# Kernel optimization log

Hardware: AMD Instinct MI355X
Metric: run time of the kernel (lower is better)

The kernel has to match this reference:

```python
import jax, jax.numpy as jnp
import numpy as np

BLOCK = 192
SCALE = 2048 ** (-0.5)


def setup_inputs() -> dict:
    key = jax.random.key(0)
    k1, k2, k3, k4 = jax.random.split(key, 4)
    B, N, C = 8, 1920, 512
    x = jax.random.normal(k1, (B, N, C), dtype=jnp.float32)
    g = jax.random.normal(k2, (B, N, C), dtype=jnp.float32)
    # nn.Linear(dim, dim, bias=False) weights, stored as [out, in] like torch
    Wq = jax.random.normal(k3, (C, C), dtype=jnp.float32) * (1.0 / np.sqrt(C))
    Wg = jax.random.normal(k4, (C, C), dtype=jnp.float32) * (1.0 / np.sqrt(C))
    return {"x": x, "g": g, "Wq": Wq, "Wg": Wg}


def reference(x, g, Wq, Wg):
    B, N, C = g.shape
    # q = x + mean over tokens of g
    q = x + jnp.mean(g, axis=1, keepdims=True)
    rel_q = jnp.einsum('bnc,dc->bnd', q, Wq)  # Linear: y = x @ W^T
    # ---- block-local cosine attention over chunks of 192 tokens ----
    gb = g.reshape(B * N // BLOCK, BLOCK, C)
    norm = jnp.linalg.norm(gb, axis=-1, keepdims=True)
    rel = gb / jnp.maximum(norm, 1e-12)  # F.normalize(dim=-1)
    scores = jnp.einsum('bic,bjc->bij', rel, rel) * SCALE  # [nb,192,192]
    attn = jax.nn.softmax(scores, axis=-1)
    g2 = jnp.einsum('bij,bjc->bic', attn, gb).reshape(B, N, C)
    # ---- global cross attention ----
    rel_g = jnp.einsum('bnc,dc->bnd', g2, Wg)
    scores2 = jnp.einsum('bmc,bnc->bmn', rel_q, rel_g) * SCALE  # [B,M,N]
    attn2 = jax.nn.softmax(scores2, axis=-1)
    out = jnp.einsum('bmn,bnc->bmc', attn2, g2)
    return out
```

## Files before the change

kernel.cpp:

```cpp
#include <hip/hip_runtime.h>
#include <math.h>

constexpr int Bsz  = 8;
constexpr int Ntok = 1920;
constexpr int Cdim = 512;
constexpr int BLK  = 192;
constexpr int Mrows = Bsz * Ntok;
constexpr int NBLK  = Mrows / BLK;
constexpr float SCALE = 0.02209708691207961f;

typedef _Float16 half8 __attribute__((ext_vector_type(8)));
typedef float    f32x4 __attribute__((ext_vector_type(4)));

#define GLOAD_LDS16(gp, lp) __builtin_amdgcn_global_load_lds( \
    (const __attribute__((address_space(1))) void*)(gp),      \
    (__attribute__((address_space(3))) void*)(lp), 16, 0, 0)

__device__ inline unsigned short f2h(float f) {
    _Float16 h = (_Float16)f;
    return __builtin_bit_cast(unsigned short, h);
}
__device__ inline float h2f(unsigned short u) {
    return (float)__builtin_bit_cast(_Float16, u);
}

template<int BK> __device__ inline int smask(int r) {
    return (BK == 32) ? ((r & 3) ^ ((r >> 2) & 3)) : (r & 7);
}

template<int N> __device__ __forceinline__ void vm_wait() {
    if constexpr (N == 0)      asm volatile("s_waitcnt vmcnt(0)" ::: "memory");
    else if constexpr (N == 2) asm volatile("s_waitcnt vmcnt(2)" ::: "memory");
    else if constexpr (N == 4) asm volatile("s_waitcnt vmcnt(4)" ::: "memory");
    else if constexpr (N == 6) asm volatile("s_waitcnt vmcnt(6)" ::: "memory");
    else                       asm volatile("s_waitcnt vmcnt(8)" ::: "memory");
}

__global__ __launch_bounds__(256) void prep_g(
    const float* __restrict__ g, unsigned short* __restrict__ gh,
    float* __restrict__ invn)
{
    int wid = threadIdx.x >> 6, lane = threadIdx.x & 63;
    int row = blockIdx.x * 4 + wid;
    const float* p = g + (size_t)row * Cdim + lane * 8;
    float4 v0 = *(const float4*)p;
    float4 v1 = *(const float4*)(p + 4);
    float ss = v0.x * v0.x + v0.y * v0.y + v0.z * v0.z + v0.w * v0.w
             + v1.x * v1.x + v1.y * v1.y + v1.z * v1.z + v1.w * v1.w;
    #pragma unroll
    for (int o = 1; o < 64; o <<= 1) ss += __shfl_xor(ss, o);
    if (lane == 0) invn[row] = 1.0f / fmaxf(sqrtf(ss), 1e-12f);
    ushort4 h0, h1;
    h0.x = f2h(v0.x); h0.y = f2h(v0.y); h0.z = f2h(v0.z); h0.w = f2h(v0.w);
    h1.x = f2h(v1.x); h1.y = f2h(v1.y); h1.z = f2h(v1.z); h1.w = f2h(v1.w);
    ushort4* d = (ushort4*)(gh + (size_t)row * Cdim + lane * 8);
    d[0] = h0; d[1] = h1;
}

__global__ void mean_partial(const unsigned short* __restrict__ gh, float* __restrict__ part) {
    int b = blockIdx.x, t = blockIdx.y, c = threadIdx.x;
    const unsigned short* p = gh + ((size_t)b * Ntok + (size_t)t * 48) * Cdim + c;
    float s = 0.f;
    #pragma unroll 4
    for (int n = 0; n < 48; ++n) s += h2f(p[(size_t)n * Cdim]);
    part[((size_t)b * 40 + t) * Cdim + c] = s;
}

__global__ void mean_final(const float* __restrict__ part, float* __restrict__ meang) {
    int b = blockIdx.x, c = threadIdx.x;
    float s = 0.f;
    for (int t = 0; t < 40; ++t) s += part[((size_t)b * 40 + t) * Cdim + c];
    meang[b * Cdim + c] = s * (1.0f / (float)Ntok);
}

__global__ void cvt_k(const float* __restrict__ src, const float* __restrict__ bias,
                      unsigned short* __restrict__ dst, int n4) {
    int i = blockIdx.x * 256 + threadIdx.x;
    if (i >= n4) return;
    float4 v = ((const float4*)src)[i];
    if (bias) {
        int b  = i / (Ntok * Cdim / 4);
        int c4 = (i & (Cdim / 4 - 1)) << 2;
        float4 bv = *(const float4*)&bias[b * Cdim + c4];
        v.x += bv.x; v.y += bv.y; v.z += bv.z; v.w += bv.w;
    }
    ushort4 h;
    h.x = f2h(v.x); h.y = f2h(v.y); h.z = f2h(v.z); h.w = f2h(v.w);
    ((ushort4*)dst)[i] = h;
}

__global__ __launch_bounds__(256) void transpose1(
    const unsigned short* __restrict__ in, unsigned short* __restrict__ out,
    int R, int C, long inB, long outB)
{
    int z = blockIdx.z;
    in  += (size_t)z * inB;
    out += (size_t)z * outB;
    __shared__ unsigned short th[64][68];
    int r0 = blockIdx.y * 64, c0 = blockIdx.x * 64;
    int tr = threadIdx.x >> 4, tc = (threadIdx.x & 15) * 4;
    for (int rr = tr; rr < 64; rr += 16) {
        ushort4 h = *(const ushort4*)&in[(size_t)(r0 + rr) * C + c0 + tc];
        th[tc + 0][rr] = h.x; th[tc + 1][rr] = h.y; th[tc + 2][rr] = h.z; th[tc + 3][rr] = h.w;
    }
    __syncthreads();
    for (int cc = tr; cc < 64; cc += 16) {
        ushort4 h = *(const ushort4*)&th[cc][tc];
        *(ushort4*)&out[(size_t)(c0 + cc) * R + r0 + tc] = h;
    }
}

template<int FM, int FN, int BK>
__global__ __launch_bounds__(256) void mfma_gemm(
    const unsigned short* __restrict__ A, const unsigned short* __restrict__ B,
    float* __restrict__ Of32, unsigned short* __restrict__ Oh,
    int N, int K, int ld,
    long aB, long bB, long oB,
    float alpha, const float* __restrict__ rs, const float* __restrict__ cs, int sB,
    float* __restrict__ psum, int pM, int pSlots)
{
    constexpr int BM = FM * 32, BN = FN * 32;
    constexpr int RPC = 512 / BK;
    constexpr int LPR = BK / 8;
    constexpr int NCH = (BM + BN) / RPC;
    constexpr int CPW = NCH / 4;
    int z = blockIdx.z;

    int gx = gridDim.x;
    int nwg = gx * gridDim.y;
    int orig = blockIdx.y * gx + blockIdx.x;
    int q = nwg >> 3, r = nwg & 7;
    int xcd = orig & 7, idx = orig >> 3;
    int wgid = (xcd < r ? xcd * (q + 1) : r * (q + 1) + (xcd - r) * q) + idx;
    int bx = wgid % gx;
    int m0 = (wgid / gx) * BM, n0 = bx * BN;

    __shared__ __align__(16) unsigned short As[2][BM * BK];
    __shared__ __align__(16) unsigned short Bs[2][BN * BK];

    int tid  = threadIdx.x;
    int lane = tid & 63, wid = tid >> 6;
    int wm = (wid >> 1) * (FM * 16), wn = (wid & 1) * (FN * 16);

    int srow = lane / LPR;
    int sgc  = (lane % LPR) ^ smask<BK>(srow);

    const unsigned short* csrc[CPW];
    unsigned short* cdst0[CPW];
    unsigned short* cdst1[CPW];
    #pragma unroll
    for (int i = 0; i < CPW; ++i) {
        int c = wid * CPW + i;
        if (c < BM / RPC) {
            csrc[i]  = A + (size_t)z * aB + (size_t)(m0 + c * RPC + srow) * ld + sgc * 8;
            cdst0[i] = &As[0][c * 512];
            cdst1[i] = &As[1][c * 512];
        } else {
            int cb = c - BM / RPC;
            csrc[i]  = B + (size_t)z * bB + (size_t)(n0 + cb * RPC + srow) * ld + sgc * 8;
            cdst0[i] = &Bs[0][cb * 512];
            cdst1[i] = &Bs[1][cb * 512];
        }
    }

    f32x4 acc[FM][FN] = {};
    int fr = lane & 15, kq = lane >> 4;

    const int nt = K / BK;
    #pragma unroll
    for (int i = 0; i < CPW; ++i) GLOAD_LDS16(csrc[i], cdst0[i]);
    #pragma unroll
    for (int i = 0; i < CPW; ++i) GLOAD_LDS16(csrc[i] + BK, cdst1[i]);

    for (int t = 0; t < nt; ++t) {
        int cur = t & 1;
        if (t + 1 < nt) vm_wait<CPW>(); else vm_wait<0>();
        __builtin_amdgcn_sched_barrier(0);
        __builtin_amdgcn_s_barrier();
        __builtin_amdgcn_sched_barrier(0);

        const unsigned short* Ab = As[cur];
        const unsigned short* Bb = Bs[cur];
        #pragma unroll
        for (int ks = 0; ks < BK / 32; ++ks) {
            int slot = ks * 4 + kq;
            half8 a[FM], b[FN];
            #pragma unroll
            for (int f = 0; f < FM; ++f) {
                int rr = wm + f * 16 + fr;
                a[f] = *(const half8*)&Ab[rr * BK + ((slot ^ smask<BK>(rr)) << 3)];
            }
            #pragma unroll
            for (int f = 0; f < FN; ++f) {
                int rr = wn + f * 16 + fr;
                b[f] = *(const half8*)&Bb[rr * BK + ((slot ^ smask<BK>(rr)) << 3)];
            }
            #pragma unroll
            for (int i = 0; i < FM; ++i)
                #pragma unroll
                for (int j = 0; j < FN; ++j)
                    acc[i][j] = __builtin_amdgcn_mfma_f32_16x16x32_f16(a[i], b[j], acc[i][j], 0, 0, 0);
        }

        __builtin_amdgcn_sched_barrier(0);
        __builtin_amdgcn_s_barrier();
        if (t + 2 < nt) {
            const int k2 = (t + 2) * BK;
            #pragma unroll
            for (int i = 0; i < CPW; ++i)
                GLOAD_LDS16(csrc[i] + k2, cur ? cdst1[i] : cdst0[i]);
        }
    }

    float* O          = Of32 ? Of32 + (size_t)z * oB : nullptr;
    unsigned short* H = Oh   ? Oh   + (size_t)z * oB : nullptr;
    int fq = lane >> 4;
    if (psum) {
        int slotB = bx * (BN / 32) + (wn >> 5);
        #pragma unroll
        for (int i = 0; i < FM; ++i) {
            #pragma unroll
            for (int r4 = 0; r4 < 4; ++r4) {
                int gm = m0 + wm + i * 16 + fq * 4 + r4;
                float rf = alpha * (rs ? rs[(size_t)z * sB + gm] : 1.0f);
                float rsum = 0.f;
                #pragma unroll
                for (int j = 0; j < FN; ++j) {
                    int gn = n0 + wn + j * 16 + fr;
                    float v = acc[i][j][r4] * rf * (cs ? cs[(size_t)z * sB + gn] : 1.0f);
                    float e = __expf(v);
                    H[(size_t)gm * N + gn] = f2h(e);
                    rsum += e;
                }
                rsum += __shfl_xor(rsum, 1);
                rsum += __shfl_xor(rsum, 2);
                rsum += __shfl_xor(rsum, 4);
                rsum += __shfl_xor(rsum, 8);
                if (fr == 0)
                    psum[((size_t)z * pM + gm) * pSlots + slotB] = rsum;
            }
        }
    } else {
        #pragma unroll
        for (int i = 0; i < FM; ++i) {
            #pragma unroll
            for (int r4 = 0; r4 < 4; ++r4) {
                int gm = m0 + wm + i * 16 + fq * 4 + r4;
                float rf = alpha * (rs ? rs[(size_t)z * sB + gm] : 1.0f);
                #pragma unroll
                for (int j = 0; j < FN; ++j) {
                    int gn = n0 + wn + j * 16 + fr;
                    float v = acc[i][j][r4] * rf * (cs ? cs[(size_t)z * sB + gn] : 1.0f);
                    size_t off = (size_t)gm * N + gn;
                    if (O) O[off] = v;
                    else   H[off] = f2h(v);
                }
            }
        }
    }
}

__global__ __launch_bounds__(512, 2) void gemm256(
    const unsigned short* __restrict__ A, const unsigned short* __restrict__ B,
    unsigned short* __restrict__ Oh, float* __restrict__ psum,
    int M, int N, int K, int ld,
    long aB, long bB, long oB, float alpha)
{
    int z = blockIdx.z;
    int gx = gridDim.x;
    int nwg = gx * gridDim.y;
    int orig = blockIdx.y * gx + blockIdx.x;
    int q = nwg >> 3, r = nwg & 7;
    int xcd = orig & 7, idx = orig >> 3;
    int wgid = (xcd < r ? xcd * (q + 1) : r * (q + 1) + (xcd - r) * q) + idx;
    int bx = wgid % gx;
    int m0 = (wgid / gx) * 256, n0 = bx * 256;

    __shared__ __align__(16) unsigned short As[2][256 * 64];
    __shared__ __align__(16) unsigned short Bs[2][256 * 64];

    int tid = threadIdx.x, lane = tid & 63, wid = tid >> 6;
    int wr = wid >> 2, wc = wid & 3;
    const unsigned short* Az = A + (size_t)z * aB;
    const unsigned short* Bz = B + (size_t)z * bB;

    int srow8 = lane >> 3;
    int sslot = (lane & 7) ^ srow8;

    auto stageT = [&](int t) {
        int cur = t & 1;
        const int koff = t * 64;
        #pragma unroll
        for (int i = 0; i < 4; ++i) {
            int c = wid * 4 + i;
            int rrow = c * 8 + srow8;
            int gr = min(m0 + rrow, M - 1);
            GLOAD_LDS16(Az + (size_t)gr * ld + koff + sslot * 8, &As[cur][c * 512]);
        }
        #pragma unroll
        for (int i = 0; i < 4; ++i) {
            int c = wid * 4 + i;
            int rrow = c * 8 + srow8;
            int gc = min(n0 + rrow, N - 1);
            GLOAD_LDS16(Bz + (size_t)gc * ld + koff + sslot * 8, &Bs[cur][c * 512]);
        }
    };

    f32x4 acc[8][4] = {};
    int fr = lane & 15, kq = lane >> 4;

    const int nt = K / 64;
    stageT(0);
    stageT(1);

    for (int t = 0; t < nt; ++t) {
        int cur = t & 1;
        if (t + 1 < nt) vm_wait<8>(); else vm_wait<0>();
        __builtin_amdgcn_sched_barrier(0);
        __builtin_amdgcn_s_barrier();
        __builtin_amdgcn_sched_barrier(0);

        const unsigned short* Ab = As[cur];
        const unsigned short* Bb = Bs[cur];
        __builtin_amdgcn_s_setprio(1);
        half8 b[4][2];
        #pragma unroll
        for (int nf = 0; nf < 4; ++nf) {
            int rr = wc * 64 + nf * 16 + fr;
            #pragma unroll
            for (int ks = 0; ks < 2; ++ks) {
                int slot = (ks * 4 + kq) ^ (rr & 7);
                b[nf][ks] = *(const half8*)&Bb[rr * 64 + slot * 8];
            }
        }
        #pragma unroll
        for (int mf = 0; mf < 8; ++mf) {
            int rr = wr * 128 + mf * 16 + fr;
            half8 a[2];
            #pragma unroll
            for (int ks = 0; ks < 2; ++ks) {
                int slot = (ks * 4 + kq) ^ (rr & 7);
                a[ks] = *(const half8*)&Ab[rr * 64 + slot * 8];
            }
            #pragma unroll
            for (int nf = 0; nf < 4; ++nf)
                #pragma unroll
                for (int ks = 0; ks < 2; ++ks)
                    acc[mf][nf] = __builtin_amdgcn_mfma_f32_16x16x32_f16(
                        a[ks], b[nf][ks], acc[mf][nf], 0, 0, 0);
        }
        __builtin_amdgcn_s_setprio(0);

        __builtin_amdgcn_sched_barrier(0);
        __builtin_amdgcn_s_barrier();
        __builtin_amdgcn_sched_barrier(0);
        if (t + 2 < nt) stageT(t + 2);
    }

    unsigned short* H = Oh + (size_t)z * oB;
    int fq = lane >> 4;
    #pragma unroll
    for (int mi = 0; mi < 8; ++mi) {
        #pragma unroll
        for (int r4 = 0; r4 < 4; ++r4) {
            int gm = m0 + wr * 128 + mi * 16 + fq * 4 + r4;
            bool vrow = gm < M;
            float rsum = 0.f;
            #pragma unroll
            for (int ni = 0; ni < 4; ++ni) {
                int gn = n0 + wc * 64 + ni * 16 + fr;
                float e = __expf(acc[mi][ni][r4] * alpha);
                if (vrow && gn < N) {
                    H[(size_t)gm * N + gn] = f2h(e);
                    rsum += e;
                }
            }
            rsum += __shfl_xor(rsum, 1);
            rsum += __shfl_xor(rsum, 2);
            rsum += __shfl_xor(rsum, 4);
            rsum += __shfl_xor(rsum, 8);
            if (vrow && fr == 0)
                psum[((size_t)z * M + gm) * 32 + bx * 4 + wc] = rsum;
        }
    }
}

__global__ void rowsum_inv(const float* __restrict__ ps, float* __restrict__ inv,
                           int rows, int slots) {
    int i = blockIdx.x * 256 + threadIdx.x;
    if (i >= rows) return;
    const float* p = ps + (size_t)i * slots;
    float s = 0.f;
    for (int j = 0; j < slots; ++j) s += p[j];
    inv[i] = 1.0f / s;
}

extern "C" void kernel_launch(void* const* d_in, const int* in_sizes, int n_in,
                              void* d_out, int out_size, void* d_ws, size_t ws_size,
                              hipStream_t stream) {
    (void)in_sizes; (void)n_in; (void)out_size; (void)ws_size;
    const float* x  = (const float*)d_in[0];
    const float* g  = (const float*)d_in[1];
    const float* Wq = (const float*)d_in[2];
    const float* Wg = (const float*)d_in[3];
    float* out = (float*)d_out;

    const size_t GE = (size_t)Mrows * Cdim;
    const size_t WE = (size_t)Cdim * Cdim;
    char* ws = (char*)d_ws;
    size_t off = 0;
    auto alloc = [&](size_t bytes) { char* p = ws + off; off += (bytes + 255) & ~(size_t)255; return p; };

    float* meang = (float*)alloc(Bsz * Cdim * 4);
    float* part  = (float*)alloc(Bsz * 40 * Cdim * 4);
    float* invn  = (float*)alloc(Mrows * 4);
    unsigned short* gh   = (unsigned short*)alloc(GE * 2);
    unsigned short* gTh  = (unsigned short*)alloc(GE * 2);
    unsigned short* qh   = (unsigned short*)alloc(GE * 2);
    unsigned short* wqh  = (unsigned short*)alloc(WE * 2);
    unsigned short* wgh  = (unsigned short*)alloc(WE * 2);
    unsigned short* wqT  = (unsigned short*)alloc(WE * 2);
    unsigned short* wgT  = (unsigned short*)alloc(WE * 2);
    unsigned short* wh   = (unsigned short*)alloc(WE * 2);
    unsigned short* qWh  = (unsigned short*)alloc(GE * 2);
    unsigned short* g2h  = (unsigned short*)alloc(GE * 2);
    unsigned short* sbh  = (unsigned short*)alloc((size_t)NBLK * BLK * BLK * 2);
    unsigned short* s2h  = (unsigned short*)alloc((size_t)Bsz * Ntok * Ntok * 2);
    float* psum   = (float*)alloc((size_t)Mrows * 32 * 4);
    float* psumb  = (float*)alloc((size_t)Mrows * 6 * 4);
    float* rsinv  = (float*)alloc((size_t)Mrows * 4);
    float* rsinvb = (float*)alloc((size_t)Mrows * 4);
    unsigned short* g2Th = qh;

    prep_g<<<Mrows / 4, 256, 0, stream>>>(g, gh, invn);

    mean_partial<<<dim3(Bsz, 40), 512, 0, stream>>>(gh, part);
    mean_final<<<Bsz, 512, 0, stream>>>(part, meang);

    cvt_k<<<(int)(GE / 4 + 255) / 256, 256, 0, stream>>>(x, meang, qh, (int)(GE / 4));
    cvt_k<<<(int)(WE / 4) / 256, 256, 0, stream>>>(Wq, nullptr, wqh, (int)(WE / 4));
    cvt_k<<<(int)(WE / 4) / 256, 256, 0, stream>>>(Wg, nullptr, wgh, (int)(WE / 4));
    transpose1<<<dim3(8, 8, 1), 256, 0, stream>>>(wqh, wqT, Cdim, Cdim, 0, 0);
    transpose1<<<dim3(8, 8, 1), 256, 0, stream>>>(wgh, wgT, Cdim, Cdim, 0, 0);

    mfma_gemm<2, 2, 64><<<dim3(8, 8), 256, 0, stream>>>(
        wgT, wqT, nullptr, wh, Cdim, Cdim, Cdim, 0, 0, 0,
        1.0f, nullptr, nullptr, 0, nullptr, 0, 0);

    transpose1<<<dim3(Cdim / 64, BLK / 64, NBLK), 256, 0, stream>>>(
        gh, gTh, BLK, Cdim, (long)BLK * Cdim, (long)Cdim * BLK);

    mfma_gemm<2, 4, 64><<<dim3(Cdim / 128, Mrows / 64), 256, 0, stream>>>(
        qh, wh, nullptr, qWh, Cdim, Cdim, Cdim, 0, 0, 0,
        1.0f, nullptr, nullptr, 0, nullptr, 0, 0);

    mfma_gemm<2, 2, 32><<<dim3(3, 3, NBLK), 256, 0, stream>>>(
        gh, gh, nullptr, sbh, BLK, Cdim, Cdim,
        (long)BLK * Cdim, (long)BLK * Cdim, (long)BLK * BLK,
        SCALE, invn, invn, BLK, psumb, BLK, 6);

    rowsum_inv<<<(Mrows + 255) / 256, 256, 0, stream>>>(psumb, rsinvb, Mrows, 6);

    mfma_gemm<2, 4, 64><<<dim3(Cdim / 128, BLK / 64, NBLK), 256, 0, stream>>>(
        sbh, gTh, nullptr, g2h, Cdim, BLK, BLK,
        (long)BLK * BLK, (long)Cdim * BLK, (long)BLK * Cdim,
        1.0f, rsinvb, nullptr, BLK, nullptr, 0, 0);

    transpose1<<<dim3(Cdim / 64, Ntok / 64, Bsz), 256, 0, stream>>>(
        g2h, g2Th, Ntok, Cdim, (long)Ntok * Cdim, (long)Cdim * Ntok);

    gemm256<<<dim3(8, 8, Bsz), 512, 0, stream>>>(
        qWh, g2h, s2h, psum, Ntok, Ntok, Cdim, Cdim,
        (long)Ntok * Cdim, (long)Ntok * Cdim, (long)Ntok * Ntok, SCALE);

    rowsum_inv<<<(Mrows + 255) / 256, 256, 0, stream>>>(psum, rsinv, Mrows, 32);

    mfma_gemm<4, 4, 64><<<dim3(Cdim / 128, Ntok / 128, Bsz), 256, 0, stream>>>(
        s2h, g2Th, out, nullptr, Cdim, Ntok, Ntok,
        (long)Ntok * Ntok, (long)Cdim * Ntok, (long)Ntok * Cdim,
        1.0f, rsinv, nullptr, Ntok, nullptr, 0, 0);
}
```

Baseline: 221.5 us.

## Fuse g2 transpose into block-attention GEMM epilogue, use exp2, retile q projection

```diff
diff --git a/kernel.cpp b/kernel.cpp
--- a/kernel.cpp
+++ b/kernel.cpp
@@ -8,6 +8,7 @@
 constexpr int Mrows = Bsz * Ntok;
 constexpr int NBLK  = Mrows / BLK;
 constexpr float SCALE = 0.02209708691207961f;
+constexpr float LOG2E = 1.4426950408889634f;
 
 typedef _Float16 half8 __attribute__((ext_vector_type(8)));
 typedef float    f32x4 __attribute__((ext_vector_type(4)));
@@ -117,7 +118,8 @@
     int N, int K, int ld,
     long aB, long bB, long oB,
     float alpha, const float* __restrict__ rs, const float* __restrict__ cs, int sB,
-    float* __restrict__ psum, int pM, int pSlots)
+    float* __restrict__ psum, int pM, int pSlots,
+    unsigned short* __restrict__ OT)
 {
     constexpr int BM = FM * 32, BN = FN * 32;
     constexpr int RPC = 512 / BK;
@@ -228,7 +230,7 @@
                 for (int j = 0; j < FN; ++j) {
                     int gn = n0 + wn + j * 16 + fr;
                     float v = acc[i][j][r4] * rf * (cs ? cs[(size_t)z * sB + gn] : 1.0f);
-                    float e = __expf(v);
+                    float e = exp2f(v);
                     H[(size_t)gm * N + gn] = f2h(e);
                     rsum += e;
                 }
@@ -252,8 +254,15 @@
                     int gn = n0 + wn + j * 16 + fr;
                     float v = acc[i][j][r4] * rf * (cs ? cs[(size_t)z * sB + gn] : 1.0f);
                     size_t off = (size_t)gm * N + gn;
+                    unsigned short hv = f2h(v);
                     if (O) O[off] = v;
-                    else   H[off] = f2h(v);
+                    else   H[off] = hv;
+                    if (OT) {
+                        int tokg = z * BLK + gm;
+                        int b    = tokg / Ntok;
+                        int tk   = tokg - b * Ntok;
+                        OT[((size_t)b * Cdim + gn) * Ntok + tk] = hv;
+                    }
                 }
             }
         }
@@ -369,7 +378,7 @@
             #pragma unroll
             for (int ni = 0; ni < 4; ++ni) {
                 int gn = n0 + wc * 64 + ni * 16 + fr;
-                float e = __expf(acc[mi][ni][r4] * alpha);
+                float e = exp2f(acc[mi][ni][r4] * alpha);
                 if (vrow && gn < N) {
                     H[(size_t)gm * N + gn] = f2h(e);
                     rsum += e;
@@ -445,38 +454,35 @@
 
     mfma_gemm<2, 2, 64><<<dim3(8, 8), 256, 0, stream>>>(
         wgT, wqT, nullptr, wh, Cdim, Cdim, Cdim, 0, 0, 0,
-        1.0f, nullptr, nullptr, 0, nullptr, 0, 0);
+        1.0f, nullptr, nullptr, 0, nullptr, 0, 0, nullptr);
 
     transpose1<<<dim3(Cdim / 64, BLK / 64, NBLK), 256, 0, stream>>>(
         gh, gTh, BLK, Cdim, (long)BLK * Cdim, (long)Cdim * BLK);
 
-    mfma_gemm<2, 4, 64><<<dim3(Cdim / 128, Mrows / 64), 256, 0, stream>>>(
+    mfma_gemm<4, 4, 64><<<dim3(Cdim / 128, Mrows / 128), 256, 0, stream>>>(
         qh, wh, nullptr, qWh, Cdim, Cdim, Cdim, 0, 0, 0,
-        1.0f, nullptr, nullptr, 0, nullptr, 0, 0);
+        1.0f, nullptr, nullptr, 0, nullptr, 0, 0, nullptr);
 
     mfma_gemm<2, 2, 32><<<dim3(3, 3, NBLK), 256, 0, stream>>>(
         gh, gh, nullptr, sbh, BLK, Cdim, Cdim,
         (long)BLK * Cdim, (long)BLK * Cdim, (long)BLK * BLK,
-        SCALE, invn, invn, BLK, psumb, BLK, 6);
+        SCALE * LOG2E, invn, invn, BLK, psumb, BLK, 6, nullptr);
 
     rowsum_inv<<<(Mrows + 255) / 256, 256, 0, stream>>>(psumb, rsinvb, Mrows, 6);
 
     mfma_gemm<2, 4, 64><<<dim3(Cdim / 128, BLK / 64, NBLK), 256, 0, stream>>>(
         sbh, gTh, nullptr, g2h, Cdim, BLK, BLK,
         (long)BLK * BLK, (long)Cdim * BLK, (long)BLK * Cdim,
-        1.0f, rsinvb, nullptr, BLK, nullptr, 0, 0);
-
-    transpose1<<<dim3(Cdim / 64, Ntok / 64, Bsz), 256, 0, stream>>>(
-        g2h, g2Th, Ntok, Cdim, (long)Ntok * Cdim, (long)Cdim * Ntok);
+        1.0f, rsinvb, nullptr, BLK, nullptr, 0, 0, g2Th);
 
     gemm256<<<dim3(8, 8, Bsz), 512, 0, stream>>>(
         qWh, g2h, s2h, psum, Ntok, Ntok, Cdim, Cdim,
-        (long)Ntok * Cdim, (long)Ntok * Cdim, (long)Ntok * Ntok, SCALE);
+        (long)Ntok * Cdim, (long)Ntok * Cdim, (long)Ntok * Ntok, SCALE * LOG2E);
 
     rowsum_inv<<<(Mrows + 255) / 256, 256, 0, stream>>>(psum, rsinv, Mrows, 32);
 
     mfma_gemm<4, 4, 64><<<dim3(Cdim / 128, Ntok / 128, Bsz), 256, 0, stream>>>(
         s2h, g2Th, out, nullptr, Cdim, Ntok, Ntok,
         (long)Ntok * Ntok, (long)Cdim * Ntok, (long)Ntok * Cdim,
-        1.0f, rsinv, nullptr, Ntok, nullptr, 0, 0);
-}
+        1.0f, rsinv, nullptr, Ntok, nullptr, 0, 0, nullptr);
+}
```

Result: slower. 238.6 us (+7.7%).
